# Kernel tuning notes

Measured on AMD Instinct MI355X. Metric: run time of the kernel, lower is better.

## Reference

```python
import jax, jax.numpy as jnp
import numpy as np

B, S, C = 8, 512, 1024
H = 16
R = 32            # lora_rank
LORA_ALPHA = 1.0  # lora scaling (alpha=1)
HID = C           # mlp_ratio = 1


def setup_inputs() -> dict:
    key = jax.random.key(0)
    ks = jax.random.split(key, 20)
    g = lambda k, shp, s=0.02: jax.random.normal(k, shp, dtype=jnp.float32) * s
    inp = {
        "x": jax.random.normal(ks[0], (B, S, C), dtype=jnp.float32),
        "mask": jax.random.randint(ks[1], (B, 3 * S), 0, 2).astype(bool),
        # qkv: Linear(dim, 3*dim, bias=False), stored [in, out]
        "qkv_w": g(ks[2], (C, 3 * C)),
        "qkv_la": g(ks[3], (C, R)),
        "qkv_lb": g(ks[4], (R, 3 * C)),
        "proj_w": g(ks[5], (C, C)),
        "proj_b": jnp.zeros((C,), jnp.float32),
        "proj_la": g(ks[6], (C, R)),
        "proj_lb": g(ks[7], (R, C)),
        "fc1_w": g(ks[8], (C, HID)),
        "fc1_b": jnp.zeros((HID,), jnp.float32),
        "fc1_la": g(ks[9], (C, R)),
        "fc1_lb": g(ks[10], (R, HID)),
        "fc2_w": g(ks[11], (HID, C)),
        "fc2_b": jnp.zeros((C,), jnp.float32),
        "fc2_la": g(ks[12], (C, R)),
        "fc2_lb": g(ks[13], (R, C)),
    }
    return inp


def reference(x, mask, qkv_w, qkv_la, qkv_lb, proj_w, proj_b, proj_la, proj_lb,
              fc1_w, fc1_b, fc1_la, fc1_lb, fc2_w, fc2_b, fc2_la, fc2_lb):
    # cross_modality='a', mask_modality='a' (constants)
    b, s, c = x.shape
    hd = c // H
    scale = hd ** (-0.5)

    # fused QKV + LoRA low-rank update
    qkv = x @ qkv_w + ((x @ qkv_la) @ qkv_lb) * LORA_ALPHA      # [B,S,3C]
    qkv = qkv.reshape(b, s, 3, H, hd).transpose(2, 0, 3, 1, 4)  # [3,B,H,S,hd]
    q, k, v = qkv[0] * scale, qkv[1], qkv[2]

    # fp32 QK^T, modality 'a' mask slice, fill -inf, softmax, NaN->0
    attn = jnp.einsum('bhqd,bhkd->bhqk',
                      q.astype(jnp.float32), k.astype(jnp.float32))
    m = mask[:, :s]                                             # 'a' slice
    attn = jnp.where(m[:, None, None, :], attn, -jnp.inf)
    attn = jax.nn.softmax(attn, axis=-1).astype(x.dtype)
    attn = jnp.where(jnp.isnan(attn), jnp.zeros((), x.dtype), attn)

    xo = jnp.einsum('bhqk,bhkd->bhqd', attn, v)                 # [B,H,S,hd]
    xo = xo.transpose(0, 2, 1, 3).reshape(b, s, c)

    # MLP (with LoRA on both fc layers); torch nn.GELU default = exact erf
    h = xo @ fc1_w + fc1_b + ((xo @ fc1_la) @ fc1_lb) * LORA_ALPHA
    h = jax.nn.gelu(h, approximate=False)
    h = h @ fc2_w + fc2_b + ((h @ fc2_la) @ fc2_lb) * LORA_ALPHA
    xo = xo + h

    out = xo @ proj_w + proj_b + ((xo @ proj_la) @ proj_lb) * LORA_ALPHA
    return out
```

## Files before the change

### kernel.cpp

```cpp
#include <hip/hip_runtime.h>

typedef _Float16 f16;
typedef _Float16 f16x8 __attribute__((ext_vector_type(8)));
typedef _Float16 f16x4v __attribute__((ext_vector_type(4)));
typedef float f32x4 __attribute__((ext_vector_type(4)));

#define DEVINL __device__ __forceinline__

DEVINL void gload16(const void* g, void* l) {
  __builtin_amdgcn_global_load_lds(
      (const __attribute__((address_space(1))) void*)g,
      (__attribute__((address_space(3))) void*)l, 16, 0, 0);
}

__global__ __launch_bounds__(256) void weff_kernel(
    const float* __restrict__ W, const float* __restrict__ la,
    const float* __restrict__ lb, f16* __restrict__ WT,
    int N, int K, int scaleCols)
{
  __shared__ float T[64][65];
  __shared__ float La[64][33];
  __shared__ float Lb[32][65];
  int n0 = blockIdx.x * 64, k0 = blockIdx.y * 64;
  int t = threadIdx.x;
  for (int i = 0; i < 16; ++i) {
    int idx = i * 256 + t; int kk = idx >> 6, nn = idx & 63;
    T[nn][kk] = W[(size_t)(k0 + kk) * N + n0 + nn];
  }
  for (int i = 0; i < 8; ++i) {
    int idx = i * 256 + t; int kk = idx >> 5, rr = idx & 31;
    La[kk][rr] = la[(size_t)(k0 + kk) * 32 + rr];
  }
  for (int i = 0; i < 8; ++i) {
    int idx = i * 256 + t; int rr = idx >> 6, nn = idx & 63;
    Lb[rr][nn] = lb[(size_t)rr * N + n0 + nn];
  }
  __syncthreads();
  for (int i = 0; i < 16; ++i) {
    int idx = i * 256 + t; int nn = idx >> 6, kk = idx & 63;
    float acc = T[nn][kk];
    #pragma unroll
    for (int r = 0; r < 32; ++r) acc += La[kk][r] * Lb[r][nn];
    if (n0 + nn < scaleCols) acc *= 0.125f;
    WT[(size_t)(n0 + nn) * K + k0 + kk] = (f16)acc;
  }
}

__global__ __launch_bounds__(256) void cvt_f32_f16(const float* __restrict__ in,
                                                   f16* __restrict__ out)
{
  int i = (blockIdx.x * 256 + threadIdx.x) * 4;
  float4 v = *(const float4*)(in + i);
  f16x4v o = {(f16)v.x, (f16)v.y, (f16)v.z, (f16)v.w};
  *(f16x4v*)(out + i) = o;
}

__global__ __launch_bounds__(256) void mask_canon(const unsigned char* __restrict__ m,
                                                  unsigned char* __restrict__ out)
{
  __shared__ int flag;
  if (threadIdx.x == 0) flag = 0;
  __syncthreads();
  int found = 0;
  for (int p = threadIdx.x; p < 12288; p += 256)
    if ((p & 3) && m[p]) found = 1;
  if (found) flag = 1;
  __syncthreads();
  int u8 = flag;
  const int* mi = (const int*)m;
  for (int idx = threadIdx.x; idx < 4096; idx += 256) {
    int b = idx >> 9, k = idx & 511;
    int v = u8 ? (int)m[b * 1536 + k] : mi[b * 1536 + k];
    out[idx] = (unsigned char)(v != 0);
  }
}

template <int EPI>
__global__ __launch_bounds__(256) void gemm128(
    const f16* __restrict__ A, const f16* __restrict__ Bt,
    int M, int N, int K,
    const float* __restrict__ bias, const f16* __restrict__ resid,
    f16* __restrict__ outH, float* __restrict__ outF,
    f16* __restrict__ Qo, f16* __restrict__ Ko, f16* __restrict__ Vto)
{
  __shared__ __align__(16) f16 As[128 * 32];
  __shared__ __align__(16) f16 Bs[128 * 32];
  int tid = threadIdx.x, wid = tid >> 6, l = tid & 63;
  int lg = l >> 4, lr = l & 15;
  int bm = blockIdx.x * 128, bn = blockIdx.y * 128;
  int wr = (wid >> 1) * 64, wc = (wid & 1) * 64;
  f32x4 acc[4][4] = {};

  const f16* gA = A + (size_t)(bm + wid * 16 + (l >> 2)) * K + (l & 3) * 8;
  const f16* gB = Bt + (size_t)(bn + wid * 16 + (l >> 2)) * K + (l & 3) * 8;
  f16* lA = As + wid * 16 * 32;
  f16* lB = Bs + wid * 16 * 32;

  for (int k0 = 0; k0 < K; k0 += 32) {
    __syncthreads();
    gload16(gA + k0, lA);
    gload16(gA + (size_t)64 * K + k0, lA + 64 * 32);
    gload16(gB + k0, lB);
    gload16(gB + (size_t)64 * K + k0, lB + 64 * 32);
    __syncthreads();
    f16x8 af[4], bf[4];
    #pragma unroll
    for (int i = 0; i < 4; ++i)
      af[i] = *(const f16x8*)(As + (wr + i * 16 + lr) * 32 + lg * 8);
    #pragma unroll
    for (int j = 0; j < 4; ++j)
      bf[j] = *(const f16x8*)(Bs + (wc + j * 16 + lr) * 32 + lg * 8);
    #pragma unroll
    for (int i = 0; i < 4; ++i)
      #pragma unroll
      for (int j = 0; j < 4; ++j)
        acc[i][j] = __builtin_amdgcn_mfma_f32_16x16x32_f16(af[i], bf[j], acc[i][j], 0, 0, 0);
  }

  #pragma unroll
  for (int i = 0; i < 4; ++i) {
    #pragma unroll
    for (int j = 0; j < 4; ++j) {
      int n = bn + wc + j * 16 + lr;
      float bv = (EPI >= 1) ? bias[n] : 0.0f;
      #pragma unroll
      for (int r = 0; r < 4; ++r) {
        int m = bm + wr + i * 16 + lg * 4 + r;
        float v = acc[i][j][r];
        if (EPI == 0) {
          int bb = m >> 9, ss = m & 511;
          int which = n >> 10, c = n & 1023, hh = c >> 6, dd = c & 63;
          size_t base = (size_t)(bb * 16 + hh);
          if (which == 0)      Qo[(base * 512 + ss) * 64 + dd] = (f16)v;
          else if (which == 1) Ko[(base * 512 + ss) * 64 + dd] = (f16)v;
          else                 Vto[(base * 64 + dd) * 512 + ss] = (f16)v;
        } else if (EPI == 1) {
          v += bv;
          v = 0.5f * v * (1.0f + erff(v * 0.70710678118654752f));
          outH[(size_t)m * N + n] = (f16)v;
        } else if (EPI == 2) {
          v += bv + (float)resid[(size_t)m * N + n];
          outH[(size_t)m * N + n] = (f16)v;
        } else {
          outF[(size_t)m * N + n] = v + bv;
        }
      }
    }
  }
}

__global__ __launch_bounds__(256) void attn_kernel(
    const f16* __restrict__ Q, const f16* __restrict__ Kc,
    const f16* __restrict__ Vt, const unsigned char* __restrict__ cmask,
    f16* __restrict__ XO)
{
  __shared__ __align__(16) f16 Ks[128 * 64];
  __shared__ __align__(16) f16 Vs[64 * 128];
  __shared__ __align__(16) f16 Ps[4 * 32 * 128];
  int tid = threadIdx.x, w = tid >> 6, l = tid & 63;
  int lg = l >> 4, lr = l & 15;
  int qblk = blockIdx.x, bh = blockIdx.y;
  int b = bh >> 4, h = bh & 15;
  const f16* Qg = Q + (size_t)bh * 512 * 64 + qblk * 128 * 64;
  const f16* Kg = Kc + (size_t)bh * 512 * 64;
  const f16* Vg = Vt + (size_t)bh * 64 * 512;
  const unsigned char* mb = cmask + b * 512;

  f16x8 qf[2][2];
  #pragma unroll
  for (int i = 0; i < 2; ++i)
    #pragma unroll
    for (int kc = 0; kc < 2; ++kc)
      qf[i][kc] = *(const f16x8*)(Qg + (size_t)(w * 32 + i * 16 + lr) * 64 + kc * 32 + lg * 8);

  f32x4 O[2][4] = {};
  float mrow[2][4], lrow[2][4];
  #pragma unroll
  for (int i = 0; i < 2; ++i)
    #pragma unroll
    for (int r = 0; r < 4; ++r) { mrow[i][r] = -1e30f; lrow[i][r] = 0.0f; }

  f16* Pw = Ps + w * 32 * 128;

  for (int kt = 0; kt < 4; ++kt) {
    __syncthreads();
    #pragma unroll
    for (int is = 0; is < 4; ++is)
      gload16(Kg + (size_t)(kt * 128 + is * 32 + w * 8 + (l >> 3)) * 64 + (l & 7) * 8,
              Ks + (is * 32 + w * 8) * 64);
    #pragma unroll
    for (int is = 0; is < 4; ++is)
      gload16(Vg + (size_t)(is * 16 + w * 4 + lg) * 512 + kt * 128 + lr * 8,
              Vs + (is * 16 + w * 4) * 128);
    __syncthreads();

    f32x4 sc[2][8] = {};
    #pragma unroll
    for (int j = 0; j < 8; ++j) {
      f16x8 kf0 = *(const f16x8*)(Ks + (j * 16 + lr) * 64 + lg * 8);
      f16x8 kf1 = *(const f16x8*)(Ks + (j * 16 + lr) * 64 + 32 + lg * 8);
      sc[0][j] = __builtin_amdgcn_mfma_f32_16x16x32_f16(qf[0][0], kf0, sc[0][j], 0, 0, 0);
      sc[0][j] = __builtin_amdgcn_mfma_f32_16x16x32_f16(qf[0][1], kf1, sc[0][j], 0, 0, 0);
      sc[1][j] = __builtin_amdgcn_mfma_f32_16x16x32_f16(qf[1][0], kf0, sc[1][j], 0, 0, 0);
      sc[1][j] = __builtin_amdgcn_mfma_f32_16x16x32_f16(qf[1][1], kf1, sc[1][j], 0, 0, 0);
    }
    bool keep[8];
    #pragma unroll
    for (int j = 0; j < 8; ++j) keep[j] = mb[kt * 128 + j * 16 + lr] != 0;
    #pragma unroll
    for (int i = 0; i < 2; ++i)
      #pragma unroll
      for (int j = 0; j < 8; ++j)
        #pragma unroll
        for (int r = 0; r < 4; ++r)
          sc[i][j][r] = keep[j] ? sc[i][j][r] : -1e30f;

    #pragma unroll
    for (int i = 0; i < 2; ++i) {
      #pragma unroll
      for (int r = 0; r < 4; ++r) {
        float pm = sc[i][0][r];
        #pragma unroll
        for (int j = 1; j < 8; ++j) pm = fmaxf(pm, sc[i][j][r]);
        pm = fmaxf(pm, __shfl_xor(pm, 1));
        pm = fmaxf(pm, __shfl_xor(pm, 2));
        pm = fmaxf(pm, __shfl_xor(pm, 4));
        pm = fmaxf(pm, __shfl_xor(pm, 8));
        float mn = fmaxf(mrow[i][r], pm);
        float alpha = __expf(mrow[i][r] - mn);
        mrow[i][r] = mn;
        lrow[i][r] *= alpha;
        #pragma unroll
        for (int jd = 0; jd < 4; ++jd) O[i][jd][r] *= alpha;
      }
    }
    #pragma unroll
    for (int i = 0; i < 2; ++i) {
      float rs[4] = {0.f, 0.f, 0.f, 0.f};
      #pragma unroll
      for (int j = 0; j < 8; ++j)
        #pragma unroll
        for (int r = 0; r < 4; ++r) {
          float p = __expf(sc[i][j][r] - mrow[i][r]);
          rs[r] += p;
          Pw[(i * 16 + lg * 4 + r) * 128 + j * 16 + lr] = (f16)p;
        }
      #pragma unroll
      for (int r = 0; r < 4; ++r) {
        float s = rs[r];
        s += __shfl_xor(s, 1); s += __shfl_xor(s, 2);
        s += __shfl_xor(s, 4); s += __shfl_xor(s, 8);
        lrow[i][r] += s;
      }
    }
    #pragma unroll
    for (int kk = 0; kk < 4; ++kk) {
      f16x8 pa0 = *(const f16x8*)(Pw + lr * 128 + kk * 32 + lg * 8);
      f16x8 pa1 = *(const f16x8*)(Pw + (16 + lr) * 128 + kk * 32 + lg * 8);
      #pragma unroll
      for (int jd = 0; jd < 4; ++jd) {
        f16x8 vb = *(const f16x8*)(Vs + (jd * 16 + lr) * 128 + kk * 32 + lg * 8);
        O[0][jd] = __builtin_amdgcn_mfma_f32_16x16x32_f16(pa0, vb, O[0][jd], 0, 0, 0);
        O[1][jd] = __builtin_amdgcn_mfma_f32_16x16x32_f16(pa1, vb, O[1][jd], 0, 0, 0);
      }
    }
  }

  #pragma unroll
  for (int i = 0; i < 2; ++i)
    #pragma unroll
    for (int r = 0; r < 4; ++r) {
      int q = qblk * 128 + w * 32 + i * 16 + lg * 4 + r;
      float inv = 1.0f / lrow[i][r];
      #pragma unroll
      for (int jd = 0; jd < 4; ++jd) {
        int c = h * 64 + jd * 16 + lr;
        XO[((size_t)b * 512 + q) * 1024 + c] = (f16)(O[i][jd][r] * inv);
      }
    }
}

extern "C" void kernel_launch(void* const* d_in, const int* in_sizes, int n_in,
                              void* d_out, int out_size, void* d_ws, size_t ws_size,
                              hipStream_t stream)
{
  (void)in_sizes; (void)n_in; (void)out_size; (void)ws_size;
  const float* x            = (const float*)d_in[0];
  const unsigned char* mask = (const unsigned char*)d_in[1];
  const float* qkv_w   = (const float*)d_in[2];
  const float* qkv_la  = (const float*)d_in[3];
  const float* qkv_lb  = (const float*)d_in[4];
  const float* proj_w  = (const float*)d_in[5];
  const float* proj_b  = (const float*)d_in[6];
  const float* proj_la = (const float*)d_in[7];
  const float* proj_lb = (const float*)d_in[8];
  const float* fc1_w   = (const float*)d_in[9];
  const float* fc1_b   = (const float*)d_in[10];
  const float* fc1_la  = (const float*)d_in[11];
  const float* fc1_lb  = (const float*)d_in[12];
  const float* fc2_w   = (const float*)d_in[13];
  const float* fc2_b   = (const float*)d_in[14];
  const float* fc2_la  = (const float*)d_in[15];
  const float* fc2_lb  = (const float*)d_in[16];
  float* out = (float*)d_out;

  f16* p = (f16*)d_ws;
  f16* WqkvT = p; p += 3072 * 1024;
  f16* W1T   = p; p += 1024 * 1024;
  f16* W2T   = p; p += 1024 * 1024;
  f16* WpT   = p; p += 1024 * 1024;
  f16* Xh    = p; p += 4096 * 1024;
  f16* Qb    = p; p += 128 * 512 * 64;
  f16* Kb    = p; p += 128 * 512 * 64;
  f16* Vt    = p; p += 128 * 64 * 512;
  f16* XO    = p; p += 4096 * 1024;
  unsigned char* cmask = (unsigned char*)p;
  f16* Hb  = Qb;
  f16* XO2 = Xh;

  weff_kernel<<<dim3(48, 16), 256, 0, stream>>>(qkv_w, qkv_la, qkv_lb, WqkvT, 3072, 1024, 1024);
  weff_kernel<<<dim3(16, 16), 256, 0, stream>>>(fc1_w, fc1_la, fc1_lb, W1T, 1024, 1024, 0);
  weff_kernel<<<dim3(16, 16), 256, 0, stream>>>(fc2_w, fc2_la, fc2_lb, W2T, 1024, 1024, 0);
  weff_kernel<<<dim3(16, 16), 256, 0, stream>>>(proj_w, proj_la, proj_lb, WpT, 1024, 1024, 0);
  cvt_f32_f16<<<4096, 256, 0, stream>>>(x, Xh);
  mask_canon<<<1, 256, 0, stream>>>(mask, cmask);

  gemm128<0><<<dim3(32, 24), 256, 0, stream>>>(Xh, WqkvT, 4096, 3072, 1024,
      nullptr, nullptr, nullptr, nullptr, Qb, Kb, Vt);
  attn_kernel<<<dim3(4, 128), 256, 0, stream>>>(Qb, Kb, Vt, cmask, XO);
  gemm128<1><<<dim3(32, 8), 256, 0, stream>>>(XO, W1T, 4096, 1024, 1024,
      fc1_b, nullptr, Hb, nullptr, nullptr, nullptr, nullptr);
  gemm128<2><<<dim3(32, 8), 256, 0, stream>>>(Hb, W2T, 4096, 1024, 1024,
      fc2_b, XO, XO2, nullptr, nullptr, nullptr, nullptr);
  gemm128<3><<<dim3(32, 8), 256, 0, stream>>>(XO2, WpT, 4096, 1024, 1024,
      proj_b, nullptr, nullptr, out, nullptr, nullptr, nullptr);
}
```

Baseline: 338.8 us.

## Swizzle LDS layouts, widen GEMM K-tile, remap workgroups, rewrite LoRA weight merge

Adds XOR swizzling to the shared-memory tiles in the GEMM and attention kernels so the 16-byte fragment reads avoid LDS bank conflicts. The GEMM K-step grows from 32 to 64, halving the barrier count per tile, and workgroup indices are remapped in both GEMM and attention for better cache locality across XCDs. The LoRA weight-merge kernel is rewritten to keep lb in registers, cover 256 columns per block, and write transposed fp16 rows through a swizzled LDS buffer with vector stores. In exchange the GEMM uses twice the LDS per block and more fragment registers, and the remap assumes the grid size is a multiple of 8.

```diff
diff --git a/kernel.cpp b/kernel.cpp
--- a/kernel.cpp
+++ b/kernel.cpp
@@ -13,36 +13,41 @@
       (__attribute__((address_space(3))) void*)l, 16, 0, 0);
 }
 
-__global__ __launch_bounds__(256) void weff_kernel(
+__global__ __launch_bounds__(256) void weff2(
     const float* __restrict__ W, const float* __restrict__ la,
     const float* __restrict__ lb, f16* __restrict__ WT,
     int N, int K, int scaleCols)
 {
-  __shared__ float T[64][65];
-  __shared__ float La[64][33];
-  __shared__ float Lb[32][65];
-  int n0 = blockIdx.x * 64, k0 = blockIdx.y * 64;
+  __shared__ __align__(16) f16 Ts[256 * 64];
   int t = threadIdx.x;
-  for (int i = 0; i < 16; ++i) {
-    int idx = i * 256 + t; int kk = idx >> 6, nn = idx & 63;
-    T[nn][kk] = W[(size_t)(k0 + kk) * N + n0 + nn];
-  }
-  for (int i = 0; i < 8; ++i) {
-    int idx = i * 256 + t; int kk = idx >> 5, rr = idx & 31;
-    La[kk][rr] = la[(size_t)(k0 + kk) * 32 + rr];
-  }
-  for (int i = 0; i < 8; ++i) {
-    int idx = i * 256 + t; int rr = idx >> 6, nn = idx & 63;
-    Lb[rr][nn] = lb[(size_t)rr * N + n0 + nn];
+  int n0 = blockIdx.x * 256, k0 = blockIdx.y * 64;
+  float scale = (n0 < scaleCols) ? 0.125f : 1.0f;
+  float lbr[32];
+  #pragma unroll
+  for (int r = 0; r < 32; ++r) lbr[r] = lb[(size_t)r * N + n0 + t];
+  #pragma unroll
+  for (int c = 0; c < 8; ++c) {
+    float acc[8];
+    #pragma unroll
+    for (int j = 0; j < 8; ++j)
+      acc[j] = W[(size_t)(k0 + c * 8 + j) * N + n0 + t];
+    #pragma unroll
+    for (int j = 0; j < 8; ++j)
+      #pragma unroll
+      for (int r = 0; r < 32; ++r)
+        acc[j] += la[(size_t)(k0 + c * 8 + j) * 32 + r] * lbr[r];
+    f16x8 h;
+    #pragma unroll
+    for (int j = 0; j < 8; ++j) h[j] = (f16)(acc[j] * scale);
+    *(f16x8*)(Ts + t * 64 + ((c ^ (t & 7)) * 8)) = h;
   }
   __syncthreads();
-  for (int i = 0; i < 16; ++i) {
-    int idx = i * 256 + t; int nn = idx >> 6, kk = idx & 63;
-    float acc = T[nn][kk];
-    #pragma unroll
-    for (int r = 0; r < 32; ++r) acc += La[kk][r] * Lb[r][nn];
-    if (n0 + nn < scaleCols) acc *= 0.125f;
-    WT[(size_t)(n0 + nn) * K + k0 + kk] = (f16)acc;
+  #pragma unroll
+  for (int it = 0; it < 8; ++it) {
+    int id = it * 256 + t;
+    int row = id >> 3, c = id & 7;
+    f16x8 h = *(const f16x8*)(Ts + row * 64 + ((c ^ (row & 7)) * 8));
+    *(f16x8*)(WT + (size_t)(n0 + row) * K + k0 + c * 8) = h;
   }
 }
 
@@ -83,38 +88,54 @@
     f16* __restrict__ outH, float* __restrict__ outF,
     f16* __restrict__ Qo, f16* __restrict__ Ko, f16* __restrict__ Vto)
 {
-  __shared__ __align__(16) f16 As[128 * 32];
-  __shared__ __align__(16) f16 Bs[128 * 32];
+  __shared__ __align__(16) f16 As[128 * 64];
+  __shared__ __align__(16) f16 Bs[128 * 64];
   int tid = threadIdx.x, wid = tid >> 6, l = tid & 63;
   int lg = l >> 4, lr = l & 15;
-  int bm = blockIdx.x * 128, bn = blockIdx.y * 128;
+  int nbx = gridDim.x;
+  int nwg = nbx * gridDim.y;
+  int flat = blockIdx.y * nbx + blockIdx.x;
+  flat = (flat & 7) * (nwg >> 3) + (flat >> 3);
+  int bm = (flat % nbx) * 128, bn = (flat / nbx) * 128;
   int wr = (wid >> 1) * 64, wc = (wid & 1) * 64;
   f32x4 acc[4][4] = {};
 
-  const f16* gA = A + (size_t)(bm + wid * 16 + (l >> 2)) * K + (l & 3) * 8;
-  const f16* gB = Bt + (size_t)(bn + wid * 16 + (l >> 2)) * K + (l & 3) * 8;
-  f16* lA = As + wid * 16 * 32;
-  f16* lB = Bs + wid * 16 * 32;
-
-  for (int k0 = 0; k0 < K; k0 += 32) {
+  int srow = l >> 3, scol = l & 7;
+  int sc8 = (scol ^ srow) * 8;
+  const f16* gA = A + (size_t)(bm + wid * 32 + srow) * K + sc8;
+  const f16* gB = Bt + (size_t)(bn + wid * 32 + srow) * K + sc8;
+  f16* lA = As + wid * 32 * 64;
+  f16* lB = Bs + wid * 32 * 64;
+
+  for (int k0 = 0; k0 < K; k0 += 64) {
     __syncthreads();
-    gload16(gA + k0, lA);
-    gload16(gA + (size_t)64 * K + k0, lA + 64 * 32);
-    gload16(gB + k0, lB);
-    gload16(gB + (size_t)64 * K + k0, lB + 64 * 32);
+    #pragma unroll
+    for (int is = 0; is < 4; ++is) {
+      gload16(gA + (size_t)(is * 8) * K + k0, lA + is * 8 * 64);
+      gload16(gB + (size_t)(is * 8) * K + k0, lB + is * 8 * 64);
+    }
     __syncthreads();
-    f16x8 af[4], bf[4];
-    #pragma unroll
-    for (int i = 0; i < 4; ++i)
-      af[i] = *(const f16x8*)(As + (wr + i * 16 + lr) * 32 + lg * 8);
-    #pragma unroll
-    for (int j = 0; j < 4; ++j)
-      bf[j] = *(const f16x8*)(Bs + (wc + j * 16 + lr) * 32 + lg * 8);
-    #pragma unroll
-    for (int i = 0; i < 4; ++i)
-      #pragma unroll
-      for (int j = 0; j < 4; ++j)
-        acc[i][j] = __builtin_amdgcn_mfma_f32_16x16x32_f16(af[i], bf[j], acc[i][j], 0, 0, 0);
+    f16x8 af[2][4], bf[2][4];
+    int x = lr & 7;
+    #pragma unroll
+    for (int i = 0; i < 4; ++i) {
+      int row = wr + i * 16 + lr;
+      af[0][i] = *(const f16x8*)(As + row * 64 + ((lg ^ x) * 8));
+      af[1][i] = *(const f16x8*)(As + row * 64 + (((4 + lg) ^ x) * 8));
+    }
+    #pragma unroll
+    for (int j = 0; j < 4; ++j) {
+      int row = wc + j * 16 + lr;
+      bf[0][j] = *(const f16x8*)(Bs + row * 64 + ((lg ^ x) * 8));
+      bf[1][j] = *(const f16x8*)(Bs + row * 64 + (((4 + lg) ^ x) * 8));
+    }
+    #pragma unroll
+    for (int kk = 0; kk < 2; ++kk)
+      #pragma unroll
+      for (int i = 0; i < 4; ++i)
+        #pragma unroll
+        for (int j = 0; j < 4; ++j)
+          acc[i][j] = __builtin_amdgcn_mfma_f32_16x16x32_f16(af[kk][i], bf[kk][j], acc[i][j], 0, 0, 0);
   }
 
   #pragma unroll
@@ -159,7 +180,9 @@
   __shared__ __align__(16) f16 Ps[4 * 32 * 128];
   int tid = threadIdx.x, w = tid >> 6, l = tid & 63;
   int lg = l >> 4, lr = l & 15;
-  int qblk = blockIdx.x, bh = blockIdx.y;
+  int flat = blockIdx.y * 4 + blockIdx.x;
+  flat = (flat & 7) * 64 + (flat >> 3);
+  int qblk = flat & 3, bh = flat >> 2;
   int b = bh >> 4, h = bh & 15;
   const f16* Qg = Q + (size_t)bh * 512 * 64 + qblk * 128 * 64;
   const f16* Kg = Kc + (size_t)bh * 512 * 64;
@@ -181,24 +204,31 @@
     for (int r = 0; r < 4; ++r) { mrow[i][r] = -1e30f; lrow[i][r] = 0.0f; }
 
   f16* Pw = Ps + w * 32 * 128;
+  int ksrow = l >> 3;
+  int ksc = ((l & 7) ^ ksrow) * 8;
+  int vrow = l >> 4;
+  int v7 = (w * 4 + vrow) & 7;
+  int vsc = ((l & 15) ^ v7) * 8;
 
   for (int kt = 0; kt < 4; ++kt) {
     __syncthreads();
     #pragma unroll
     for (int is = 0; is < 4; ++is)
-      gload16(Kg + (size_t)(kt * 128 + is * 32 + w * 8 + (l >> 3)) * 64 + (l & 7) * 8,
+      gload16(Kg + (size_t)(kt * 128 + is * 32 + w * 8 + ksrow) * 64 + ksc,
               Ks + (is * 32 + w * 8) * 64);
     #pragma unroll
     for (int is = 0; is < 4; ++is)
-      gload16(Vg + (size_t)(is * 16 + w * 4 + lg) * 512 + kt * 128 + lr * 8,
+      gload16(Vg + (size_t)(is * 16 + w * 4 + vrow) * 512 + kt * 128 + vsc,
               Vs + (is * 16 + w * 4) * 128);
     __syncthreads();
 
+    int x = lr & 7;
     f32x4 sc[2][8] = {};
     #pragma unroll
     for (int j = 0; j < 8; ++j) {
-      f16x8 kf0 = *(const f16x8*)(Ks + (j * 16 + lr) * 64 + lg * 8);
-      f16x8 kf1 = *(const f16x8*)(Ks + (j * 16 + lr) * 64 + 32 + lg * 8);
+      const f16* krow = Ks + (j * 16 + lr) * 64;
+      f16x8 kf0 = *(const f16x8*)(krow + ((lg ^ x) * 8));
+      f16x8 kf1 = *(const f16x8*)(krow + (((4 + lg) ^ x) * 8));
       sc[0][j] = __builtin_amdgcn_mfma_f32_16x16x32_f16(qf[0][0], kf0, sc[0][j], 0, 0, 0);
       sc[0][j] = __builtin_amdgcn_mfma_f32_16x16x32_f16(qf[0][1], kf1, sc[0][j], 0, 0, 0);
       sc[1][j] = __builtin_amdgcn_mfma_f32_16x16x32_f16(qf[1][0], kf0, sc[1][j], 0, 0, 0);
@@ -243,7 +273,9 @@
         for (int r = 0; r < 4; ++r) {
           float p = __expf(sc[i][j][r] - mrow[i][r]);
           rs[r] += p;
-          Pw[(i * 16 + lg * 4 + r) * 128 + j * 16 + lr] = (f16)p;
+          int prow = i * 16 + lg * 4 + r;
+          int pc = j * 16 + lr;
+          Pw[prow * 128 + ((((pc >> 3) ^ (prow & 7)) << 3) | (pc & 7))] = (f16)p;
         }
       #pragma unroll
       for (int r = 0; r < 4; ++r) {
@@ -255,11 +287,12 @@
     }
     #pragma unroll
     for (int kk = 0; kk < 4; ++kk) {
-      f16x8 pa0 = *(const f16x8*)(Pw + lr * 128 + kk * 32 + lg * 8);
-      f16x8 pa1 = *(const f16x8*)(Pw + (16 + lr) * 128 + kk * 32 + lg * 8);
+      int c0 = ((kk * 4 + lg) ^ x) * 8;
+      f16x8 pa0 = *(const f16x8*)(Pw + lr * 128 + c0);
+      f16x8 pa1 = *(const f16x8*)(Pw + (16 + lr) * 128 + c0);
       #pragma unroll
       for (int jd = 0; jd < 4; ++jd) {
-        f16x8 vb = *(const f16x8*)(Vs + (jd * 16 + lr) * 128 + kk * 32 + lg * 8);
+        f16x8 vb = *(const f16x8*)(Vs + (jd * 16 + lr) * 128 + c0);
         O[0][jd] = __builtin_amdgcn_mfma_f32_16x16x32_f16(pa0, vb, O[0][jd], 0, 0, 0);
         O[1][jd] = __builtin_amdgcn_mfma_f32_16x16x32_f16(pa1, vb, O[1][jd], 0, 0, 0);
       }
@@ -318,10 +351,10 @@
   f16* Hb  = Qb;
   f16* XO2 = Xh;
 
-  weff_kernel<<<dim3(48, 16), 256, 0, stream>>>(qkv_w, qkv_la, qkv_lb, WqkvT, 3072, 1024, 1024);
-  weff_kernel<<<dim3(16, 16), 256, 0, stream>>>(fc1_w, fc1_la, fc1_lb, W1T, 1024, 1024, 0);
-  weff_kernel<<<dim3(16, 16), 256, 0, stream>>>(fc2_w, fc2_la, fc2_lb, W2T, 1024, 1024, 0);
-  weff_kernel<<<dim3(16, 16), 256, 0, stream>>>(proj_w, proj_la, proj_lb, WpT, 1024, 1024, 0);
+  weff2<<<dim3(12, 16), 256, 0, stream>>>(qkv_w, qkv_la, qkv_lb, WqkvT, 3072, 1024, 1024);
+  weff2<<<dim3(4, 16), 256, 0, stream>>>(fc1_w, fc1_la, fc1_lb, W1T, 1024, 1024, 0);
+  weff2<<<dim3(4, 16), 256, 0, stream>>>(fc2_w, fc2_la, fc2_lb, W2T, 1024, 1024, 0);
+  weff2<<<dim3(4, 16), 256, 0, stream>>>(proj_w, proj_la, proj_lb, WpT, 1024, 1024, 0);
   cvt_f32_f16<<<4096, 256, 0, stream>>>(x, Xh);
   mask_canon<<<1, 256, 0, stream>>>(mask, cmask);
 
```

New measurement: 521.8 us. +54.0%, slower.
